# Kernel tuning notes

Hardware: AMD Instinct MI355X
Metric: run time of the kernel (lower is better)

The kernel has to match this reference:

```python
import jax, jax.numpy as jnp
import numpy as np

HID = 1024
DEPTH = 2

def _rhn_layer(x, Win, bin_, Wh, bh, Wt, bt):
    # x: [B, T, in]; returns outputs [B, T, H]
    B = x.shape[0]
    h0 = jnp.zeros((B, HID), dtype=x.dtype)
    xt = jnp.swapaxes(x, 0, 1)  # [T, B, in]

    def step(h_prev, x_t):
        h = x_t @ Win + bin_
        for i in range(DEPTH):
            t_gate = jax.nn.sigmoid(h @ Wt[i] + bt[i])
            h_layer = jnp.tanh(h @ Wh[i] + bh[i])
            h = t_gate * h_layer + (1.0 - t_gate) * h
        h_new = h + h_prev
        return h_new, h_new

    _, outs = jax.lax.scan(step, h0, xt)  # [T, B, H]
    return jnp.swapaxes(outs, 0, 1)


def setup_inputs() -> dict:
    key = jax.random.key(0)
    ks = jax.random.split(key, 16)
    B, T, IN, H, OUT = 64, 256, 128, HID, 128
    s = lambda fan_in: 1.0 / np.sqrt(fan_in)
    d = {}
    d["x"] = jax.random.normal(ks[0], (B, T, IN), dtype=jnp.float32)
    # layer 0 (input_size=IN)
    d["l0_Win"] = jax.random.uniform(ks[1], (IN, H), minval=-s(IN), maxval=s(IN))
    d["l0_bin"] = jax.random.uniform(ks[2], (H,), minval=-s(IN), maxval=s(IN))
    d["l0_Wh"] = jax.random.uniform(ks[3], (DEPTH, H, H), minval=-s(H), maxval=s(H))
    d["l0_bh"] = jax.random.uniform(ks[4], (DEPTH, H), minval=-s(H), maxval=s(H))
    d["l0_Wt"] = jax.random.uniform(ks[5], (DEPTH, H, H), minval=-s(H), maxval=s(H))
    d["l0_bt"] = jax.random.uniform(ks[6], (DEPTH, H), minval=-s(H), maxval=s(H))
    # layer 1 (input_size=H)
    d["l1_Win"] = jax.random.uniform(ks[7], (H, H), minval=-s(H), maxval=s(H))
    d["l1_bin"] = jax.random.uniform(ks[8], (H,), minval=-s(H), maxval=s(H))
    d["l1_Wh"] = jax.random.uniform(ks[9], (DEPTH, H, H), minval=-s(H), maxval=s(H))
    d["l1_bh"] = jax.random.uniform(ks[10], (DEPTH, H), minval=-s(H), maxval=s(H))
    d["l1_Wt"] = jax.random.uniform(ks[11], (DEPTH, H, H), minval=-s(H), maxval=s(H))
    d["l1_bt"] = jax.random.uniform(ks[12], (DEPTH, H), minval=-s(H), maxval=s(H))
    # final fc
    d["fc_W"] = jax.random.uniform(ks[13], (H, OUT), minval=-s(H), maxval=s(H))
    d["fc_b"] = jax.random.uniform(ks[14], (OUT,), minval=-s(H), maxval=s(H))
    return d


def reference(x, l0_Win, l0_bin, l0_Wh, l0_bh, l0_Wt, l0_bt,
              l1_Win, l1_bin, l1_Wh, l1_bh, l1_Wt, l1_bt, fc_W, fc_b):
    out = _rhn_layer(x, l0_Win, l0_bin, l0_Wh, l0_bh, l0_Wt, l0_bt)
    out = _rhn_layer(out, l1_Win, l1_bin, l1_Wh, l1_bh, l1_Wt, l1_bt)
    # forecast_horizon = 1 -> last time step only
    out = out[:, -1:, :] @ fc_W + fc_b  # [B, 1, OUT]
    return out
```

## Files before the change

### kernel.cpp

```cpp
#include <hip/hip_runtime.h>

typedef unsigned short u16;
typedef unsigned int u32;
typedef __bf16 bf16x8 __attribute__((ext_vector_type(8)));
typedef float floatx4 __attribute__((ext_vector_type(4)));

#define HID 1024
#define BATCH 64
#define SEQ 256
#define INDIM 128
#define OUTDIM 128
#define MROWS (BATCH*SEQ)

__device__ __forceinline__ float b2f(u16 u) {
    union { u32 u; float f; } v; v.u = ((u32)u) << 16; return v.f;
}
__device__ __forceinline__ u16 f2b(float f) {
    union { float f; u32 u; } v; v.f = f;
    u32 x = v.u;
    x += 0x7fffu + ((x >> 16) & 1u);
    return (u16)(x >> 16);
}
__device__ __forceinline__ float sigm(float x) { return 1.f / (1.f + __expf(-x)); }
__device__ __forceinline__ float tanh_f(float x) { return 2.f / (1.f + __expf(-2.f * x)) - 1.f; }

__device__ __forceinline__ void gld16(const u16* g, u16* l) {
    __builtin_amdgcn_global_load_lds(
        (const __attribute__((address_space(1))) void*)g,
        (__attribute__((address_space(3))) void*)l, 16, 0, 0);
}

__global__ void detect_dtype(const u16* __restrict__ w, int* __restrict__ flag) {
    __shared__ int s;
    if (threadIdx.x == 0) s = 0;
    __syncthreads();
    int bad = 0;
    for (int i = threadIdx.x; i < 4096; i += 256) {
        int e = (w[i] >> 7) & 0xff;
        if (e >= 127) bad = 1;
    }
    if (bad) atomicOr(&s, 1);
    __syncthreads();
    if (threadIdx.x == 0) *flag = s;
}

struct CvtList { const void* s[7]; u16* d[7]; int n[7]; };

__global__ void convert7(CvtList C, const int* __restrict__ flag) {
    const int fp32 = *flag;
    const int z = blockIdx.y;
    const int n = C.n[z];
    const int stride = gridDim.x * 256;
    for (int i = blockIdx.x * 256 + threadIdx.x; i < n; i += stride) {
        u16 o;
        if (fp32) o = f2b(((const float*)C.s[z])[i]);
        else      o = ((const u16*)C.s[z])[i];
        C.d[z][i] = o;
    }
}

struct TListO {
    const void* s[10];
    u16*        d[10];
    int         R[10];
    int         Cc[10];
    long        off[10];
};

__global__ void transpose10(TListO L, const int* __restrict__ flag) {
    const int fp32 = *flag;
    const int z = blockIdx.z;
    const void* src = L.s[z];
    u16*        dst = L.d[z];
    const int R  = L.R[z];
    const int Cc = L.Cc[z];
    const long zo = L.off[z];
    const int tr = blockIdx.y * 32, tc = blockIdx.x * 32;
    if (tr >= R || tc >= Cc) return;
    __align__(16) __shared__ u16 t[32][33];
    const int tx = threadIdx.x, ty = threadIdx.y;
#pragma unroll
    for (int i = 0; i < 4; ++i) {
        const int r = ty + i * 8;
        const long e = zo + (long)(tr + r) * Cc + tc + tx;
        u16 v;
        if (fp32) v = f2b(((const float*)src)[e]);
        else      v = ((const u16*)src)[e];
        t[r][tx] = v;
    }
    __syncthreads();
#pragma unroll
    for (int i = 0; i < 4; ++i) {
        const int r = ty + i * 8;
        dst[(size_t)(tc + r) * R + tr + tx] = t[tx][r];
    }
}

__device__ __forceinline__ void tile_swizzle(int& m0, int& n0) {
    const int lin = blockIdx.y * gridDim.x + blockIdx.x;
    const int xcd = lin & 7;
    const int loc = lin >> 3;
    m0 = (xcd * 16 + (loc & 15)) * 128;
    n0 = (loc >> 4) * 128;
}

__global__ __launch_bounds__(256, 2) void gemm128(
    const u16* __restrict__ A, const u16* __restrict__ BT,
    const u16* __restrict__ bias, u16* __restrict__ C,
    int M, int N, int K)
{
    __align__(16) __shared__ u16 As[128 * 64];
    __align__(16) __shared__ u16 Bs[128 * 64];

    const int tid  = threadIdx.x;
    const int lane = tid & 63;
    const int wid  = tid >> 6;
    const int wr   = wid >> 1;
    const int wc   = wid & 1;

    int m0, n0;
    tile_swizzle(m0, n0);

    floatx4 acc[4][4] = {};

    const int srow = lane >> 3;
    const int scol = 8 * ((lane & 7) ^ (lane >> 3));
    const int cb   = wid * 4;
    const u16* Ag[4]; const u16* Bg[4];
    u16 *Al[4], *Bl[4];
#pragma unroll
    for (int j = 0; j < 4; ++j) {
        const int c = cb + j;
        const int r = c * 8 + srow;
        Ag[j] = A  + (size_t)(m0 + r) * K + scol;
        Bg[j] = BT + (size_t)(n0 + r) * K + scol;
        Al[j] = As + c * 512;
        Bl[j] = Bs + c * 512;
    }

    const int quad = lane >> 4;
    const int l16  = lane & 15;
    const int swz  = l16 & 7;

    const int nk = K >> 6;
    for (int kt = 0; kt < nk; ++kt) {
        __syncthreads();
#pragma unroll
        for (int j = 0; j < 4; ++j) {
            gld16(Ag[j], Al[j]);  gld16(Bg[j], Bl[j]);
            Ag[j] += 64; Bg[j] += 64;
        }
        __syncthreads();

#pragma unroll
        for (int kk = 0; kk < 2; ++kk) {
            const int slot = ((kk * 4 + quad) ^ swz) * 8;
            bf16x8 af[4], bfr[4];
#pragma unroll
            for (int i = 0; i < 4; ++i) {
                af[i]  = *(const bf16x8*)(As + (wr * 64 + i * 16 + l16) * 64 + slot);
                bfr[i] = *(const bf16x8*)(Bs + (wc * 64 + i * 16 + l16) * 64 + slot);
            }
#pragma unroll
            for (int i = 0; i < 4; ++i)
#pragma unroll
                for (int j = 0; j < 4; ++j)
                    acc[i][j] = __builtin_amdgcn_mfma_f32_16x16x32_bf16(af[i], bfr[j], acc[i][j], 0, 0, 0);
        }
    }

#pragma unroll
    for (int i = 0; i < 4; ++i) {
        const int rowb = m0 + wr * 64 + i * 16 + quad * 4;
#pragma unroll
        for (int j = 0; j < 4; ++j) {
            const int col = n0 + wc * 64 + j * 16 + l16;
            const float bv = b2f(bias[col]);
#pragma unroll
            for (int r = 0; r < 4; ++r)
                C[(size_t)(rowb + r) * N + col] = f2b(acc[i][j][r] + bv);
        }
    }
}

__global__ __launch_bounds__(256, 2) void gemm_hw(
    const u16* __restrict__ A,
    const u16* __restrict__ WtT,
    const u16* __restrict__ WhT,
    const u16* __restrict__ bt, const u16* __restrict__ bh,
    u16* __restrict__ Hout,
    int M, int N, int K)
{
    __align__(16) __shared__ u16 As [128 * 64];
    __align__(16) __shared__ u16 Bts[128 * 64];
    __align__(16) __shared__ u16 Bhs[128 * 64];

    const int tid  = threadIdx.x;
    const int lane = tid & 63;
    const int wid  = tid >> 6;
    const int wr   = wid >> 1;
    const int wc   = wid & 1;

    int m0, n0;
    tile_swizzle(m0, n0);

    floatx4 acct[4][4] = {};
    floatx4 acch[4][4] = {};

    const int srow = lane >> 3;
    const int scol = 8 * ((lane & 7) ^ (lane >> 3));
    const int cb   = wid * 4;
    const u16* Ag[4]; const u16* Tg[4]; const u16* Hg[4];
    u16 *Al[4], *Tl[4], *Hl[4];
#pragma unroll
    for (int j = 0; j < 4; ++j) {
        const int c = cb + j;
        const int r = c * 8 + srow;
        Ag[j] = A   + (size_t)(m0 + r) * K + scol;
        Tg[j] = WtT + (size_t)(n0 + r) * K + scol;
        Hg[j] = WhT + (size_t)(n0 + r) * K + scol;
        Al[j] = As  + c * 512;
        Tl[j] = Bts + c * 512;
        Hl[j] = Bhs + c * 512;
    }

    const int quad = lane >> 4;
    const int l16  = lane & 15;
    const int swz  = l16 & 7;

    const int nk = K >> 6;
    for (int kt = 0; kt < nk; ++kt) {
        __syncthreads();
#pragma unroll
        for (int j = 0; j < 4; ++j) {
            gld16(Ag[j], Al[j]);  gld16(Tg[j], Tl[j]);  gld16(Hg[j], Hl[j]);
            Ag[j] += 64; Tg[j] += 64; Hg[j] += 64;
        }
        __syncthreads();

#pragma unroll
        for (int kk = 0; kk < 2; ++kk) {
            const int slot = ((kk * 4 + quad) ^ swz) * 8;
            bf16x8 af[4], btf[4], bhf[4];
#pragma unroll
            for (int i = 0; i < 4; ++i) {
                af[i]  = *(const bf16x8*)(As  + (wr * 64 + i * 16 + l16) * 64 + slot);
                btf[i] = *(const bf16x8*)(Bts + (wc * 64 + i * 16 + l16) * 64 + slot);
                bhf[i] = *(const bf16x8*)(Bhs + (wc * 64 + i * 16 + l16) * 64 + slot);
            }
#pragma unroll
            for (int i = 0; i < 4; ++i)
#pragma unroll
                for (int j = 0; j < 4; ++j) {
                    acct[i][j] = __builtin_amdgcn_mfma_f32_16x16x32_bf16(af[i], btf[j], acct[i][j], 0, 0, 0);
                    acch[i][j] = __builtin_amdgcn_mfma_f32_16x16x32_bf16(af[i], bhf[j], acch[i][j], 0, 0, 0);
                }
        }
    }

#pragma unroll
    for (int i = 0; i < 4; ++i) {
        const int rowb = m0 + wr * 64 + i * 16 + quad * 4;
#pragma unroll
        for (int j = 0; j < 4; ++j) {
            const int col = n0 + wc * 64 + j * 16 + l16;
            const float btv = b2f(bt[col]);
            const float bhv = b2f(bh[col]);
#pragma unroll
            for (int r = 0; r < 4; ++r) {
                const size_t idx = (size_t)(rowb + r) * N + col;
                const float hold = b2f(A[idx]);
                const float tg = sigm(acct[i][j][r] + btv);
                const float hl = tanh_f(acch[i][j][r] + bhv);
                Hout[idx] = f2b(hold + tg * (hl - hold));
            }
        }
    }
}

__global__ void cumsum_t(u16* g) {
    const int id = blockIdx.x * 256 + threadIdx.x;
    const int b = id >> 10, f = id & 1023;
    size_t base = (size_t)b * SEQ * HID + f;
    float acc = 0.f;
#pragma unroll 4
    for (int t = 0; t < SEQ; ++t) {
        size_t idx = base + (size_t)t * HID;
        acc += b2f(g[idx]);
        g[idx] = f2b(acc);
    }
}

__global__ void sum_t(const u16* __restrict__ g, float* __restrict__ out) {
    const int id = blockIdx.x * 256 + threadIdx.x;
    const int b = id >> 10, f = id & 1023;
    size_t base = (size_t)b * SEQ * HID + f;
    float acc = 0.f;
#pragma unroll 4
    for (int t = 0; t < SEQ; ++t)
        acc += b2f(g[base + (size_t)t * HID]);
    out[id] = acc;
}

__global__ void fc_final(const float* __restrict__ hf, const void* __restrict__ W,
                         const void* __restrict__ bias, void* __restrict__ out,
                         const int* __restrict__ flag) {
    __shared__ float sh[HID];
    const int fp32 = *flag;
    const int b = blockIdx.x, o = threadIdx.x;
    for (int k = o; k < HID; k += 128) sh[k] = hf[(size_t)b * HID + k];
    __syncthreads();
    float acc;
    if (fp32) {
        acc = ((const float*)bias)[o];
        for (int k = 0; k < HID; ++k)
            acc += sh[k] * ((const float*)W)[(size_t)k * OUTDIM + o];
        ((float*)out)[b * OUTDIM + o] = acc;
    } else {
        acc = b2f(((const u16*)bias)[o]);
        for (int k = 0; k < HID; ++k)
            acc += sh[k] * b2f(((const u16*)W)[(size_t)k * OUTDIM + o]);
        ((u16*)out)[b * OUTDIM + o] = f2b(acc);
    }
}

extern "C" void kernel_launch(void* const* d_in, const int* in_sizes, int n_in,
                              void* d_out, int out_size, void* d_ws, size_t ws_size,
                              hipStream_t stream) {
    const void* x      = d_in[0];
    const void* l0_Win = d_in[1];
    const void* l0_bin = d_in[2];
    const void* l0_Wh  = d_in[3];
    const void* l0_bh  = d_in[4];
    const void* l0_Wt  = d_in[5];
    const void* l0_bt  = d_in[6];
    const void* l1_Win = d_in[7];
    const void* l1_bin = d_in[8];
    const void* l1_Wh  = d_in[9];
    const void* l1_bh  = d_in[10];
    const void* l1_Wt  = d_in[11];
    const void* l1_bt  = d_in[12];
    const void* fc_W   = d_in[13];
    const void* fc_b   = d_in[14];

    char* ws = (char*)d_ws;
    u16* Pa = (u16*)(ws);
    u16* Pb = (u16*)(ws + 33554432);
    u16* xc = Pb;
    u16* tW = (u16*)(ws + 67108864);
    u16* tWin0 = tW;
    u16* tWt00 = tWin0 + 131072;
    u16* tWt01 = tWt00 + 1048576;
    u16* tWh00 = tWt01 + 1048576;
    u16* tWh01 = tWh00 + 1048576;
    u16* tWin1 = tWh01 + 1048576;
    u16* tWt10 = tWin1 + 1048576;
    u16* tWt11 = tWt10 + 1048576;
    u16* tWh10 = tWt11 + 1048576;
    u16* tWh11 = tWh10 + 1048576;
    u16* smallb = tWh11 + 1048576;
    u16* binc0 = smallb;
    u16* bhc0  = binc0 + 1024;
    u16* btc0  = bhc0 + 2048;
    u16* binc1 = btc0 + 2048;
    u16* bhc1  = binc1 + 1024;
    u16* btc1  = bhc1 + 2048;
    int* flag  = (int*)(btc1 + 2048);
    float* hfinal = (float*)Pa;

    detect_dtype<<<1, 256, 0, stream>>>((const u16*)l0_Wh, flag);

    const long DD = (long)HID * HID;
    TListO L;
    L.s[0] = l0_Win; L.d[0] = tWin0; L.R[0] = INDIM; L.Cc[0] = HID; L.off[0] = 0;
    L.s[1] = l0_Wt;  L.d[1] = tWt00; L.R[1] = HID;   L.Cc[1] = HID; L.off[1] = 0;
    L.s[2] = l0_Wt;  L.d[2] = tWt01; L.R[2] = HID;   L.Cc[2] = HID; L.off[2] = DD;
    L.s[3] = l0_Wh;  L.d[3] = tWh00; L.R[3] = HID;   L.Cc[3] = HID; L.off[3] = 0;
    L.s[4] = l0_Wh;  L.d[4] = tWh01; L.R[4] = HID;   L.Cc[4] = HID; L.off[4] = DD;
    L.s[5] = l1_Win; L.d[5] = tWin1; L.R[5] = HID;   L.Cc[5] = HID; L.off[5] = 0;
    L.s[6] = l1_Wt;  L.d[6] = tWt10; L.R[6] = HID;   L.Cc[6] = HID; L.off[6] = 0;
    L.s[7] = l1_Wt;  L.d[7] = tWt11; L.R[7] = HID;   L.Cc[7] = HID; L.off[7] = DD;
    L.s[8] = l1_Wh;  L.d[8] = tWh10; L.R[8] = HID;   L.Cc[8] = HID; L.off[8] = 0;
    L.s[9] = l1_Wh;  L.d[9] = tWh11; L.R[9] = HID;   L.Cc[9] = HID; L.off[9] = DD;
    transpose10<<<dim3(32, 32, 10), dim3(32, 8), 0, stream>>>(L, flag);

    CvtList C7;
    C7.s[0] = x;      C7.d[0] = xc;    C7.n[0] = MROWS * INDIM;
    C7.s[1] = l0_bin; C7.d[1] = binc0; C7.n[1] = HID;
    C7.s[2] = l0_bh;  C7.d[2] = bhc0;  C7.n[2] = 2 * HID;
    C7.s[3] = l0_bt;  C7.d[3] = btc0;  C7.n[3] = 2 * HID;
    C7.s[4] = l1_bin; C7.d[4] = binc1; C7.n[4] = HID;
    C7.s[5] = l1_bh;  C7.d[5] = bhc1;  C7.n[5] = 2 * HID;
    C7.s[6] = l1_bt;  C7.d[6] = btc1;  C7.n[6] = 2 * HID;
    convert7<<<dim3(512, 7), 256, 0, stream>>>(C7, flag);

    gemm128<<<dim3(8, 128), 256, 0, stream>>>(xc, tWin0, binc0, Pa, MROWS, HID, INDIM);
    gemm_hw<<<dim3(8, 128), 256, 0, stream>>>(Pa, tWt00, tWh00, btc0, bhc0, Pb, MROWS, HID, HID);
    gemm_hw<<<dim3(8, 128), 256, 0, stream>>>(Pb, tWt01, tWh01, btc0 + HID, bhc0 + HID, Pa, MROWS, HID, HID);
    cumsum_t<<<256, 256, 0, stream>>>(Pa);

    gemm128<<<dim3(8, 128), 256, 0, stream>>>(Pa, tWin1, binc1, Pb, MROWS, HID, HID);
    gemm_hw<<<dim3(8, 128), 256, 0, stream>>>(Pb, tWt10, tWh10, btc1, bhc1, Pa, MROWS, HID, HID);
    gemm_hw<<<dim3(8, 128), 256, 0, stream>>>(Pa, tWt11, tWh11, btc1 + HID, bhc1 + HID, Pb, MROWS, HID, HID);

    sum_t<<<256, 256, 0, stream>>>(Pb, hfinal);
    fc_final<<<64, 128, 0, stream>>>(hfinal, fc_W, fc_b, d_out, flag);
}
```

Measured before the change: 513.6 us.

## Shrink gemm_hw tile to 128x64 with 4x1 warp layout for higher occupancy

The fused gate GEMM now uses 128x64 output tiles (each warp owns 32 rows by 64 cols) instead of 128x128, halving the accumulator registers and the B-operand shared memory. The launch bound rises to 3 blocks per SM, the grid doubles to 16x128, and a new XCD-aware block-to-tile mapping replaces tile_swizzle. The goal is more resident waves to hide the latency of the synchronous load-then-compute loop. The cost is that every A tile is reloaded twice as often, and each warp gets less MFMA work per LDS read.

```diff
diff --git a/kernel.cpp b/kernel.cpp
--- a/kernel.cpp
+++ b/kernel.cpp
@@ -183,7 +183,7 @@
     }
 }
 
-__global__ __launch_bounds__(256, 2) void gemm_hw(
+__global__ __launch_bounds__(256, 3) void gemm_hw(
     const u16* __restrict__ A,
     const u16* __restrict__ WtT,
     const u16* __restrict__ WhT,
@@ -192,34 +192,37 @@
     int M, int N, int K)
 {
     __align__(16) __shared__ u16 As [128 * 64];
-    __align__(16) __shared__ u16 Bts[128 * 64];
-    __align__(16) __shared__ u16 Bhs[128 * 64];
+    __align__(16) __shared__ u16 Bts[64 * 64];
+    __align__(16) __shared__ u16 Bhs[64 * 64];
 
     const int tid  = threadIdx.x;
     const int lane = tid & 63;
     const int wid  = tid >> 6;
-    const int wr   = wid >> 1;
-    const int wc   = wid & 1;
-
-    int m0, n0;
-    tile_swizzle(m0, n0);
-
-    floatx4 acct[4][4] = {};
-    floatx4 acch[4][4] = {};
+
+    const int lin = blockIdx.y * gridDim.x + blockIdx.x;
+    const int xcd = lin & 7;
+    const int loc = lin >> 3;
+    const int m0 = (xcd * 16 + (loc & 15)) * 128;
+    const int n0 = (loc >> 4) * 64;
+
+    floatx4 acct[2][4] = {};
+    floatx4 acch[2][4] = {};
 
     const int srow = lane >> 3;
     const int scol = 8 * ((lane & 7) ^ (lane >> 3));
-    const int cb   = wid * 4;
-    const u16* Ag[4]; const u16* Tg[4]; const u16* Hg[4];
-    u16 *Al[4], *Tl[4], *Hl[4];
+    const u16* Ag[4]; const u16* Tg[2]; const u16* Hg[2];
+    u16 *Al[4], *Tl[2], *Hl[2];
 #pragma unroll
     for (int j = 0; j < 4; ++j) {
-        const int c = cb + j;
-        const int r = c * 8 + srow;
-        Ag[j] = A   + (size_t)(m0 + r) * K + scol;
-        Tg[j] = WtT + (size_t)(n0 + r) * K + scol;
-        Hg[j] = WhT + (size_t)(n0 + r) * K + scol;
-        Al[j] = As  + c * 512;
+        const int c = wid * 4 + j;
+        Ag[j] = A + (size_t)(m0 + c * 8 + srow) * K + scol;
+        Al[j] = As + c * 512;
+    }
+#pragma unroll
+    for (int j = 0; j < 2; ++j) {
+        const int c = wid * 2 + j;
+        Tg[j] = WtT + (size_t)(n0 + c * 8 + srow) * K + scol;
+        Hg[j] = WhT + (size_t)(n0 + c * 8 + srow) * K + scol;
         Tl[j] = Bts + c * 512;
         Hl[j] = Bhs + c * 512;
     }
@@ -232,24 +235,28 @@
     for (int kt = 0; kt < nk; ++kt) {
         __syncthreads();
 #pragma unroll
-        for (int j = 0; j < 4; ++j) {
-            gld16(Ag[j], Al[j]);  gld16(Tg[j], Tl[j]);  gld16(Hg[j], Hl[j]);
-            Ag[j] += 64; Tg[j] += 64; Hg[j] += 64;
+        for (int j = 0; j < 4; ++j) { gld16(Ag[j], Al[j]); Ag[j] += 64; }
+#pragma unroll
+        for (int j = 0; j < 2; ++j) {
+            gld16(Tg[j], Tl[j]); Tg[j] += 64;
+            gld16(Hg[j], Hl[j]); Hg[j] += 64;
         }
         __syncthreads();
 
 #pragma unroll
         for (int kk = 0; kk < 2; ++kk) {
             const int slot = ((kk * 4 + quad) ^ swz) * 8;
-            bf16x8 af[4], btf[4], bhf[4];
-#pragma unroll
-            for (int i = 0; i < 4; ++i) {
-                af[i]  = *(const bf16x8*)(As  + (wr * 64 + i * 16 + l16) * 64 + slot);
-                btf[i] = *(const bf16x8*)(Bts + (wc * 64 + i * 16 + l16) * 64 + slot);
-                bhf[i] = *(const bf16x8*)(Bhs + (wc * 64 + i * 16 + l16) * 64 + slot);
+            bf16x8 af[2], btf[4], bhf[4];
+#pragma unroll
+            for (int i = 0; i < 2; ++i)
+                af[i] = *(const bf16x8*)(As + (wid * 32 + i * 16 + l16) * 64 + slot);
+#pragma unroll
+            for (int j = 0; j < 4; ++j) {
+                btf[j] = *(const bf16x8*)(Bts + (j * 16 + l16) * 64 + slot);
+                bhf[j] = *(const bf16x8*)(Bhs + (j * 16 + l16) * 64 + slot);
             }
 #pragma unroll
-            for (int i = 0; i < 4; ++i)
+            for (int i = 0; i < 2; ++i)
 #pragma unroll
                 for (int j = 0; j < 4; ++j) {
                     acct[i][j] = __builtin_amdgcn_mfma_f32_16x16x32_bf16(af[i], btf[j], acct[i][j], 0, 0, 0);
@@ -259,11 +266,11 @@
     }
 
 #pragma unroll
-    for (int i = 0; i < 4; ++i) {
-        const int rowb = m0 + wr * 64 + i * 16 + quad * 4;
+    for (int i = 0; i < 2; ++i) {
+        const int rowb = m0 + wid * 32 + i * 16 + quad * 4;
 #pragma unroll
         for (int j = 0; j < 4; ++j) {
-            const int col = n0 + wc * 64 + j * 16 + l16;
+            const int col = n0 + j * 16 + l16;
             const float btv = b2f(bt[col]);
             const float bhv = b2f(bh[col]);
 #pragma unroll
@@ -395,13 +402,13 @@
     convert7<<<dim3(512, 7), 256, 0, stream>>>(C7, flag);
 
     gemm128<<<dim3(8, 128), 256, 0, stream>>>(xc, tWin0, binc0, Pa, MROWS, HID, INDIM);
-    gemm_hw<<<dim3(8, 128), 256, 0, stream>>>(Pa, tWt00, tWh00, btc0, bhc0, Pb, MROWS, HID, HID);
-    gemm_hw<<<dim3(8, 128), 256, 0, stream>>>(Pb, tWt01, tWh01, btc0 + HID, bhc0 + HID, Pa, MROWS, HID, HID);
+    gemm_hw<<<dim3(16, 128), 256, 0, stream>>>(Pa, tWt00, tWh00, btc0, bhc0, Pb, MROWS, HID, HID);
+    gemm_hw<<<dim3(16, 128), 256, 0, stream>>>(Pb, tWt01, tWh01, btc0 + HID, bhc0 + HID, Pa, MROWS, HID, HID);
     cumsum_t<<<256, 256, 0, stream>>>(Pa);
 
     gemm128<<<dim3(8, 128), 256, 0, stream>>>(Pa, tWin1, binc1, Pb, MROWS, HID, HID);
-    gemm_hw<<<dim3(8, 128), 256, 0, stream>>>(Pb, tWt10, tWh10, btc1, bhc1, Pa, MROWS, HID, HID);
-    gemm_hw<<<dim3(8, 128), 256, 0, stream>>>(Pa, tWt11, tWh11, btc1 + HID, bhc1 + HID, Pb, MROWS, HID, HID);
+    gemm_hw<<<dim3(16, 128), 256, 0, stream>>>(Pb, tWt10, tWh10, btc1, bhc1, Pa, MROWS, HID, HID);
+    gemm_hw<<<dim3(16, 128), 256, 0, stream>>>(Pa, tWt11, tWh11, btc1 + HID, bhc1 + HID, Pb, MROWS, HID, HID);
 
     sum_t<<<256, 256, 0, stream>>>(Pb, hfinal);
     fc_final<<<64, 128, 0, stream>>>(hfinal, fc_W, fc_b, d_out, flag);
```

Result: slower. 523.9 us (+2.0%).

## Merge prep kernels, inline dtype probe, and split time cumsum into two-pass scan

Applied to the files above, without the earlier changes.

Fuses the dtype detection, weight transposes and bias/input conversion into one prep_all launch, with each wave probing the dtype via a ballot instead of reading a flag written by a separate kernel. Replaces the serial 256-step per-feature cumsum (only 256 blocks) with a chunked two-pass scan over 4 time chunks, giving four times as many threads. The cost is an extra pass that reads the activation tensor again plus a small partial-sum buffer. It also removes two kernel launches.

```diff
diff --git a/kernel.cpp b/kernel.cpp
--- a/kernel.cpp
+++ b/kernel.cpp
@@ -30,48 +30,39 @@
         (__attribute__((address_space(3))) void*)l, 16, 0, 0);
 }
 
-__global__ void detect_dtype(const u16* __restrict__ w, int* __restrict__ flag) {
-    __shared__ int s;
-    if (threadIdx.x == 0) s = 0;
-    __syncthreads();
-    int bad = 0;
-    for (int i = threadIdx.x; i < 4096; i += 256) {
-        int e = (w[i] >> 7) & 0xff;
-        if (e >= 127) bad = 1;
-    }
-    if (bad) atomicOr(&s, 1);
-    __syncthreads();
-    if (threadIdx.x == 0) *flag = s;
-}
-
-struct CvtList { const void* s[7]; u16* d[7]; int n[7]; };
-
-__global__ void convert7(CvtList C, const int* __restrict__ flag) {
-    const int fp32 = *flag;
-    const int z = blockIdx.y;
-    const int n = C.n[z];
-    const int stride = gridDim.x * 256;
-    for (int i = blockIdx.x * 256 + threadIdx.x; i < n; i += stride) {
-        u16 o;
-        if (fp32) o = f2b(((const float*)C.s[z])[i]);
-        else      o = ((const u16*)C.s[z])[i];
-        C.d[z][i] = o;
-    }
-}
-
-struct TListO {
-    const void* s[10];
-    u16*        d[10];
-    int         R[10];
-    int         Cc[10];
-    long        off[10];
+__device__ __forceinline__ int is_fp32(const u16* probe) {
+    const int lane = threadIdx.x & 63;
+    const int e = (probe[lane * 7] >> 7) & 0xff;
+    return __ballot(e >= 127) != 0ULL;
+}
+
+struct PrepList {
+    const void* s[17];
+    u16*        d[17];
+    int         R[17];
+    int         Cc[17];
+    long        off[17];
+    const u16*  probe;
 };
 
-__global__ void transpose10(TListO L, const int* __restrict__ flag) {
-    const int fp32 = *flag;
+__global__ void prep_all(PrepList L) {
+    const int fp32 = is_fp32(L.probe);
     const int z = blockIdx.z;
     const void* src = L.s[z];
     u16*        dst = L.d[z];
+    if (z >= 10) {
+        const int n = L.R[z];
+        const int tid = threadIdx.y * 32 + threadIdx.x;
+        const int blk = blockIdx.y * 32 + blockIdx.x;
+        const int stride = 1024 * 256;
+        for (int i = blk * 256 + tid; i < n; i += stride) {
+            u16 o;
+            if (fp32) o = f2b(((const float*)src)[i]);
+            else      o = ((const u16*)src)[i];
+            dst[i] = o;
+        }
+        return;
+    }
     const int R  = L.R[z];
     const int Cc = L.Cc[z];
     const long zo = L.off[z];
@@ -278,16 +269,29 @@
     }
 }
 
-__global__ void cumsum_t(u16* g) {
+__global__ void scan_pass1(const u16* __restrict__ g, float* __restrict__ partial) {
     const int id = blockIdx.x * 256 + threadIdx.x;
-    const int b = id >> 10, f = id & 1023;
-    size_t base = (size_t)b * SEQ * HID + f;
-    float acc = 0.f;
+    const int f = id & 1023, c = (id >> 10) & 3, b = id >> 12;
+    size_t base = (size_t)b * SEQ * HID + (size_t)c * 64 * HID + f;
+    float s = 0.f;
 #pragma unroll 4
-    for (int t = 0; t < SEQ; ++t) {
+    for (int t = 0; t < 64; ++t)
+        s += b2f(g[base + (size_t)t * HID]);
+    partial[id] = s;
+}
+
+__global__ void scan_pass2(u16* __restrict__ g, const float* __restrict__ partial) {
+    const int id = blockIdx.x * 256 + threadIdx.x;
+    const int f = id & 1023, c = (id >> 10) & 3, b = id >> 12;
+    float run = 0.f;
+    for (int cc = 0; cc < c; ++cc)
+        run += partial[(b << 12) + (cc << 10) + f];
+    size_t base = (size_t)b * SEQ * HID + (size_t)c * 64 * HID + f;
+#pragma unroll 4
+    for (int t = 0; t < 64; ++t) {
         size_t idx = base + (size_t)t * HID;
-        acc += b2f(g[idx]);
-        g[idx] = f2b(acc);
+        run += b2f(g[idx]);
+        g[idx] = f2b(run);
     }
 }
 
@@ -303,10 +307,9 @@
 }
 
 __global__ void fc_final(const float* __restrict__ hf, const void* __restrict__ W,
-                         const void* __restrict__ bias, void* __restrict__ out,
-                         const int* __restrict__ flag) {
+                         const void* __restrict__ bias, void* __restrict__ out) {
     __shared__ float sh[HID];
-    const int fp32 = *flag;
+    const int fp32 = is_fp32((const u16*)W);
     const int b = blockIdx.x, o = threadIdx.x;
     for (int k = o; k < HID; k += 128) sh[k] = hf[(size_t)b * HID + k];
     __syncthreads();
@@ -365,13 +368,10 @@
     u16* binc1 = btc0 + 2048;
     u16* bhc1  = binc1 + 1024;
     u16* btc1  = bhc1 + 2048;
-    int* flag  = (int*)(btc1 + 2048);
     float* hfinal = (float*)Pa;
 
-    detect_dtype<<<1, 256, 0, stream>>>((const u16*)l0_Wh, flag);
-
     const long DD = (long)HID * HID;
-    TListO L;
+    PrepList L;
     L.s[0] = l0_Win; L.d[0] = tWin0; L.R[0] = INDIM; L.Cc[0] = HID; L.off[0] = 0;
     L.s[1] = l0_Wt;  L.d[1] = tWt00; L.R[1] = HID;   L.Cc[1] = HID; L.off[1] = 0;
     L.s[2] = l0_Wt;  L.d[2] = tWt01; L.R[2] = HID;   L.Cc[2] = HID; L.off[2] = DD;
@@ -382,27 +382,27 @@
     L.s[7] = l1_Wt;  L.d[7] = tWt11; L.R[7] = HID;   L.Cc[7] = HID; L.off[7] = DD;
     L.s[8] = l1_Wh;  L.d[8] = tWh10; L.R[8] = HID;   L.Cc[8] = HID; L.off[8] = 0;
     L.s[9] = l1_Wh;  L.d[9] = tWh11; L.R[9] = HID;   L.Cc[9] = HID; L.off[9] = DD;
-    transpose10<<<dim3(32, 32, 10), dim3(32, 8), 0, stream>>>(L, flag);
-
-    CvtList C7;
-    C7.s[0] = x;      C7.d[0] = xc;    C7.n[0] = MROWS * INDIM;
-    C7.s[1] = l0_bin; C7.d[1] = binc0; C7.n[1] = HID;
-    C7.s[2] = l0_bh;  C7.d[2] = bhc0;  C7.n[2] = 2 * HID;
-    C7.s[3] = l0_bt;  C7.d[3] = btc0;  C7.n[3] = 2 * HID;
-    C7.s[4] = l1_bin; C7.d[4] = binc1; C7.n[4] = HID;
-    C7.s[5] = l1_bh;  C7.d[5] = bhc1;  C7.n[5] = 2 * HID;
-    C7.s[6] = l1_bt;  C7.d[6] = btc1;  C7.n[6] = 2 * HID;
-    convert7<<<dim3(512, 7), 256, 0, stream>>>(C7, flag);
+    L.s[10] = x;      L.d[10] = xc;    L.R[10] = MROWS * INDIM; L.Cc[10] = 0; L.off[10] = 0;
+    L.s[11] = l0_bin; L.d[11] = binc0; L.R[11] = HID;     L.Cc[11] = 0; L.off[11] = 0;
+    L.s[12] = l0_bh;  L.d[12] = bhc0;  L.R[12] = 2 * HID; L.Cc[12] = 0; L.off[12] = 0;
+    L.s[13] = l0_bt;  L.d[13] = btc0;  L.R[13] = 2 * HID; L.Cc[13] = 0; L.off[13] = 0;
+    L.s[14] = l1_bin; L.d[14] = binc1; L.R[14] = HID;     L.Cc[14] = 0; L.off[14] = 0;
+    L.s[15] = l1_bh;  L.d[15] = bhc1;  L.R[15] = 2 * HID; L.Cc[15] = 0; L.off[15] = 0;
+    L.s[16] = l1_bt;  L.d[16] = btc1;  L.R[16] = 2 * HID; L.Cc[16] = 0; L.off[16] = 0;
+    L.probe = (const u16*)l0_Wh;
+
+    prep_all<<<dim3(32, 32, 17), dim3(32, 8), 0, stream>>>(L);
 
     gemm128<<<dim3(8, 128), 256, 0, stream>>>(xc, tWin0, binc0, Pa, MROWS, HID, INDIM);
     gemm_hw<<<dim3(8, 128), 256, 0, stream>>>(Pa, tWt00, tWh00, btc0, bhc0, Pb, MROWS, HID, HID);
     gemm_hw<<<dim3(8, 128), 256, 0, stream>>>(Pb, tWt01, tWh01, btc0 + HID, bhc0 + HID, Pa, MROWS, HID, HID);
-    cumsum_t<<<256, 256, 0, stream>>>(Pa);
+    scan_pass1<<<1024, 256, 0, stream>>>(Pa, (float*)Pb);
+    scan_pass2<<<1024, 256, 0, stream>>>(Pa, (const float*)Pb);
 
     gemm128<<<dim3(8, 128), 256, 0, stream>>>(Pa, tWin1, binc1, Pb, MROWS, HID, HID);
     gemm_hw<<<dim3(8, 128), 256, 0, stream>>>(Pb, tWt10, tWh10, btc1, bhc1, Pa, MROWS, HID, HID);
     gemm_hw<<<dim3(8, 128), 256, 0, stream>>>(Pa, tWt11, tWh11, btc1 + HID, bhc1 + HID, Pb, MROWS, HID, HID);
 
     sum_t<<<256, 256, 0, stream>>>(Pb, hfinal);
-    fc_final<<<64, 128, 0, stream>>>(hfinal, fc_W, fc_b, d_out, flag);
-}
+    fc_final<<<64, 128, 0, stream>>>(hfinal, fc_W, fc_b, d_out);
+}
```

After: 540.7 us. +5.3%, slower.
